# Optimization experiments

Hardware: AMD Instinct MI355X
Metric: run time of the kernel (lower is better)

Reference implementation:

```python
import math
import jax, jax.numpy as jnp
import numpy as np

B, C, T, H, FC, L, K, S, O = 4, 512, 2048, 8, 2048, 6, 3, 256, 1
DK = C // H


def _conv1x1(x, w, b):
    # x: (B,Cin,T), w: (Cout,Cin)
    return jnp.einsum('oc,bct->bot', w, x) + b[None, :, None]


def _conv1d(x, w, b, pad):
    # x: (B,Cin,T), w: (Cout,Cin,K), pad: (left,right)
    y = jax.lax.conv_general_dilated(x, w, (1,), [pad],
                                     dimension_numbers=('NCH', 'OIH', 'NCH'))
    return y + b[None, :, None]


def _layernorm_c(x, g, b, eps=1e-5):
    # LayerNorm over channel dim (module transposes to put channels last)
    m = jnp.mean(x, axis=1, keepdims=True)
    v = jnp.mean((x - m) ** 2, axis=1, keepdims=True)
    return (x - m) * jax.lax.rsqrt(v + eps) * g[None, :, None] + b[None, :, None]


def _attention(x, qw, qb, kw, kb, vw, vb, ow, ob, tri):
    b_, c, t = x.shape
    # reshape(b, H, dk, t).transpose(2,3) -> (B,H,T,dk)
    q = _conv1x1(x, qw, qb).reshape(b_, H, DK, t).transpose(0, 1, 3, 2)
    k = _conv1x1(x, kw, kb).reshape(b_, H, DK, t).transpose(0, 1, 3, 2)
    v = _conv1x1(x, vw, vb).reshape(b_, H, DK, t).transpose(0, 1, 3, 2)
    scores = jnp.einsum('bhtd,bhsd->bhts', q, k) / math.sqrt(DK)
    scores = jnp.where(tri, scores, -1e4)  # causal mask, matches Tensor.where(mask, s, -10000)
    p = jax.nn.softmax(scores, axis=-1)
    o = jnp.einsum('bhts,bhsd->bhtd', p, v)
    o = o.transpose(0, 1, 3, 2).reshape(b_, c, t)
    return _conv1x1(o, ow, ob)


def _ffn(x, x_mask, w1, b1, w2, b2):
    # causal FFN: left pad K-1, activation=None -> relu, p_dropout=0
    y = _conv1d(x * x_mask, w1, b1, (K - 1, 0))
    y = jax.nn.relu(y)
    return _conv1d(y * x_mask, w2, b2, (K - 1, 0)) * x_mask


def _forward(x, norm_f0, x_mask, spk_emb,
             prenet_w, prenet_b, f0pre_w, f0pre_b, cond_w, cond_b, proj_w, proj_b,
             qw, qb, kw, kb, vw, vb, ow, ob,
             ln0_g, ln0_b, ln1_g, ln1_b,
             ffn1_w, ffn1_b, ffn2_w, ffn2_b):
    x = jax.lax.stop_gradient(x)  # torch.detach(x)
    x = x + _conv1x1(spk_emb, cond_w, cond_b)
    x = x + _conv1d(norm_f0, f0pre_w, f0pre_b, (1, 1))
    x = _conv1d(x, prenet_w, prenet_b, (1, 1)) * x_mask
    t = x.shape[2]
    tri = jnp.tril(jnp.ones((t, t), dtype=bool))[None, None]  # subsequent_mask
    x = x * x_mask
    for i in range(L):
        y = _attention(x, qw[i], qb[i], kw[i], kb[i], vw[i], vb[i], ow[i], ob[i], tri)
        x = _layernorm_c(x + y, ln0_g[i], ln0_b[i])
        y = _ffn(x, x_mask, ffn1_w[i], ffn1_b[i], ffn2_w[i], ffn2_b[i])
        x = _layernorm_c(x + y, ln1_g[i], ln1_b[i])
    x = x * x_mask
    return _conv1x1(x, proj_w, proj_b) * x_mask


def setup_inputs() -> dict:
    key = jax.random.key(0)
    ks = iter(jax.random.split(key, 40))
    rn = lambda shape, scale: jax.random.normal(next(ks), shape, jnp.float32) * scale
    inp = {
        'x': rn((B, C, T), 1.0),
        'norm_f0': rn((B, 1, T), 1.0),
        'x_mask': jnp.ones((B, 1, T), jnp.float32),
        'spk_emb': rn((B, S, T), 1.0),
        'prenet_w': rn((C, C, K), (C * K) ** -0.5), 'prenet_b': jnp.zeros((C,), jnp.float32),
        'f0pre_w': rn((C, 1, K), K ** -0.5), 'f0pre_b': jnp.zeros((C,), jnp.float32),
        'cond_w': rn((C, S), S ** -0.5), 'cond_b': jnp.zeros((C,), jnp.float32),
        'proj_w': rn((O, C), C ** -0.5), 'proj_b': jnp.zeros((O,), jnp.float32),
        'qw': rn((L, C, C), C ** -0.5), 'qb': jnp.zeros((L, C), jnp.float32),
        'kw': rn((L, C, C), C ** -0.5), 'kb': jnp.zeros((L, C), jnp.float32),
        'vw': rn((L, C, C), C ** -0.5), 'vb': jnp.zeros((L, C), jnp.float32),
        'ow': rn((L, C, C), C ** -0.5), 'ob': jnp.zeros((L, C), jnp.float32),
        'ln0_g': jnp.ones((L, C), jnp.float32), 'ln0_b': jnp.zeros((L, C), jnp.float32),
        'ln1_g': jnp.ones((L, C), jnp.float32), 'ln1_b': jnp.zeros((L, C), jnp.float32),
        'ffn1_w': rn((L, FC, C, K), (C * K) ** -0.5), 'ffn1_b': jnp.zeros((L, FC), jnp.float32),
        'ffn2_w': rn((L, C, FC, K), (FC * K) ** -0.5), 'ffn2_b': jnp.zeros((L, C), jnp.float32),
    }
    return inp


def reference(x, norm_f0, x_mask, spk_emb,
              prenet_w, prenet_b, f0pre_w, f0pre_b, cond_w, cond_b, proj_w, proj_b,
              qw, qb, kw, kb, vw, vb, ow, ob,
              ln0_g, ln0_b, ln1_g, ln1_b,
              ffn1_w, ffn1_b, ffn2_w, ffn2_b):
    return _forward(x, norm_f0, x_mask, spk_emb,
                    prenet_w, prenet_b, f0pre_w, f0pre_b, cond_w, cond_b, proj_w, proj_b,
                    qw, qb, kw, kb, vw, vb, ow, ob,
                    ln0_g, ln0_b, ln1_g, ln1_b,
                    ffn1_w, ffn1_b, ffn2_w, ffn2_b)
```

## Files before the change

### kernel.cpp

```cpp
#include <hip/hip_runtime.h>
#include <cstdint>
#include <cstddef>

#define T_LEN 2048
#define B_SZ 4
#define C_CH 512
#define H_N 8
#define DK_ 64
#define FC_CH 2048
#define L_N 6
#define KW 3
#define S_CH 256

typedef _Float16 h8 __attribute__((ext_vector_type(8)));
typedef _Float16 h4 __attribute__((ext_vector_type(4)));
typedef float floatx4 __attribute__((ext_vector_type(4)));

__global__ __launch_bounds__(256)
void cast_f16(const float* __restrict__ src, _Float16* __restrict__ dst, int n)
{
    int i = blockIdx.x * 256 + threadIdx.x;
    if (i < n) dst[i] = (_Float16)src[i];
}

__global__ __launch_bounds__(256)
void prepack_k3(const float* __restrict__ src, _Float16* __restrict__ dst, int rk)
{
    const int o = blockIdx.x * 256 + threadIdx.x;
    if (o >= rk) return;
    const size_t row = blockIdx.y;
    const int blk = o / 96, rr = o - blk * 96;
    const int k = rr >> 5, cl = rr & 31;
    dst[row * rk + o] = (_Float16)src[row * rk + (size_t)(blk * 32 + cl) * 3 + k];
}

__global__ __launch_bounds__(256)
void prepack_qkv(const float* __restrict__ qw, const float* __restrict__ kw,
                 const float* __restrict__ vw, const float* __restrict__ qb,
                 const float* __restrict__ kb, const float* __restrict__ vb,
                 _Float16* __restrict__ dst, float* __restrict__ bdst)
{
    int i = blockIdx.x * 256 + threadIdx.x;
    const int total = L_N * 1536 * 512;
    if (i < total) {
        int l = i / (1536 * 512);
        int o = i - l * (1536 * 512);
        int m = o >> 9, c = o & 511;
        const float* s = (m < 512) ? qw : ((m < 1024) ? kw : vw);
        dst[i] = (_Float16)s[((size_t)l * 512 + (m & 511)) * 512 + c];
    }
    if (i < L_N * 1536) {
        int l = i / 1536, m = i - l * 1536;
        const float* s = (m < 512) ? qb : ((m < 1024) ? kb : vb);
        bdst[i] = s[l * 512 + (m & 511)];
    }
}

__global__ __launch_bounds__(256)
void transpose_f0(const float* __restrict__ src, _Float16* __restrict__ dst, int Cd,
                  const float* __restrict__ nf0, const float* __restrict__ f0w,
                  const float* __restrict__ f0b, int do_f0)
{
    __shared__ float tile[32][33];
    const int tl = threadIdx.x & 31;
    const int r  = threadIdx.x >> 5;
    const int t00 = blockIdx.x * 32;
    const int c00 = blockIdx.y * 32;
    const int b   = blockIdx.z;
    const float* s0 = src + (size_t)b * Cd * T_LEN;
#pragma unroll
    for (int rr = 0; rr < 4; ++rr) {
        int cl = r + rr * 8;
        tile[cl][tl] = s0[(size_t)(c00 + cl) * T_LEN + t00 + tl];
    }
    __syncthreads();
    _Float16* d0 = dst + (size_t)b * T_LEN * Cd;
    const int cg = c00 + tl;
#pragma unroll
    for (int rr = 0; rr < 4; ++rr) {
        int tlo = r + rr * 8;
        float v = tile[tl][tlo];
        if (do_f0) {
            int tg = t00 + tlo;
            float a = f0b[cg];
#pragma unroll
            for (int k = 0; k < 3; ++k) {
                int gt = tg + k - 1;
                if (gt >= 0 && gt < T_LEN) a += f0w[cg * 3 + k] * nf0[(size_t)b * T_LEN + gt];
            }
            v += a;
        }
        d0[(size_t)(t00 + tlo) * Cd + cg] = (_Float16)v;
    }
}

template<int KK, int OUTMODE, int MT>
__global__ __launch_bounds__(256)
void conv_gemm_mfma(const _Float16* __restrict__ in, const _Float16* __restrict__ Wpk,
                    const float* __restrict__ bias, const _Float16* __restrict__ res,
                    const float* __restrict__ mask, _Float16* __restrict__ out_v,
                    _Float16* __restrict__ out2,
                    int Cin, int out_stride, int pl, int do_relu,
                    int mask_in, int mask_out)
{
    constexpr int CS   = (KK == 3) ? 32 : 64;
    constexpr int NSEC = (KK == 3) ? 3 : 2;
    constexpr int AST  = NSEC * 32 + 8;
    constexpr int HALO = (KK == 3) ? 2 : 0;
    constexpr int RB   = 128 + 2 * HALO;
    constexpr int BST  = CS + 8;
    constexpr int NAH  = NSEC * MT / 64;
    constexpr int SEGW = NSEC * MT / 8;
    constexpr int IM_N = MT / 32;
    constexpr int NTASK = RB * (CS / 16);
    __shared__ _Float16 sA[2][MT * AST];
    __shared__ _Float16 sB[2][RB * BST];

    const int tid = threadIdx.x;
    const int lane = tid & 63;
    const int wid = tid >> 6;
    const int wm = wid >> 1, wt = wid & 1;
    const int r = lane & 15, q4 = lane >> 4;
    const int t0 = blockIdx.x * 128;
    const int m0 = blockIdx.y * MT;
    const int b  = blockIdx.z;
    const float* mk = mask + (size_t)b * T_LEN;

    floatx4 acc[IM_N][4];
#pragma unroll
    for (int i = 0; i < IM_N; ++i)
#pragma unroll
        for (int j = 0; j < 4; ++j)
#pragma unroll
            for (int c = 0; c < 4; ++c) acc[i][j][c] = 0.f;

    const int arow = tid & (MT - 1);
    const int ah0  = (tid / MT) * SEGW;
    const _Float16* ap = Wpk + (size_t)(m0 + arow) * Cin * KK + ah0;

    int brw[2], bcc[2];
    bool bex[2], bval[2];
    _Float16 bm[2];
    const _Float16* bq[2];
    h8 areg[NAH], breg0[2][2], breg1[2][2];
#pragma unroll
    for (int t2 = 0; t2 < 2; ++t2) {
        const int id = tid + t2 * 256;
        bex[t2] = (id < NTASK);
        int row, c16;
        if (KK == 3) { row = id % RB; c16 = (id / RB) * 16; }
        else         { row = id >> 2; c16 = (id & 3) * 16; }
        const int gt = t0 + row - HALO;
        bval[t2] = bex[t2] && gt >= 0 && gt < T_LEN;
        brw[t2] = row; bcc[t2] = c16;
        bm[t2] = (_Float16)((bval[t2] && mask_in) ? mk[gt] : 1.f);
        bq[t2] = in + (size_t)b * T_LEN * Cin + (size_t)gt * Cin + c16;
#pragma unroll
        for (int hh = 0; hh < 2; ++hh)
#pragma unroll
            for (int j = 0; j < 8; ++j) {
                breg0[t2][hh][j] = (_Float16)0.f;
                breg1[t2][hh][j] = (_Float16)0.f;
            }
    }
    const int nch = Cin / CS;

    auto loadA = [&]() {
        ap += CS * KK;
#pragma unroll
        for (int j = 0; j < NAH; ++j) areg[j] = *reinterpret_cast<const h8*>(ap + j * 8);
    };
    auto loadB = [&](h8 (&br)[2][2]) {
#pragma unroll
        for (int t2 = 0; t2 < 2; ++t2)
            if (bval[t2]) {
                br[t2][0] = *reinterpret_cast<const h8*>(bq[t2]);
                br[t2][1] = *reinterpret_cast<const h8*>(bq[t2] + 8);
                bq[t2] += CS;
            }
    };
    auto stage = [&](int pb, h8 (&br)[2][2]) {
#pragma unroll
        for (int j = 0; j < NAH; ++j)
            *reinterpret_cast<h8*>(&sA[pb][arow * AST + ah0 + j * 8]) = areg[j];
#pragma unroll
        for (int t2 = 0; t2 < 2; ++t2)
            if (bex[t2]) {
                *reinterpret_cast<h8*>(&sB[pb][brw[t2] * BST + bcc[t2]]) = br[t2][0] * bm[t2];
                *reinterpret_cast<h8*>(&sB[pb][brw[t2] * BST + bcc[t2] + 8]) = br[t2][1] * bm[t2];
            }
    };

#pragma unroll
    for (int j = 0; j < NAH; ++j) areg[j] = *reinterpret_cast<const h8*>(ap + j * 8);
#pragma unroll
    for (int t2 = 0; t2 < 2; ++t2)
        if (bval[t2]) {
            breg0[t2][0] = *reinterpret_cast<const h8*>(bq[t2]);
            breg0[t2][1] = *reinterpret_cast<const h8*>(bq[t2] + 8);
            breg1[t2][0] = *reinterpret_cast<const h8*>(bq[t2] + CS);
            breg1[t2][1] = *reinterpret_cast<const h8*>(bq[t2] + CS + 8);
            bq[t2] += 2 * CS;
        }
    stage(0, breg0);
    loadA();
    loadB(breg0);
    __syncthreads();

    auto body = [&](int pb, int cc, h8 (&br)[2][2]) {
        h8 af0[IM_N], bf0[4];
#pragma unroll
        for (int im = 0; im < IM_N; ++im)
            af0[im] = *reinterpret_cast<const h8*>(&sA[pb][(wm * (MT / 2) + im * 16 + r) * AST + q4 * 8]);
        {
            const int rb0 = (KK == 3) ? (wt * 64 + r - pl + HALO) : (wt * 64 + r);
#pragma unroll
            for (int jt = 0; jt < 4; ++jt)
                bf0[jt] = *reinterpret_cast<const h8*>(&sB[pb][(rb0 + jt * 16) * BST + q4 * 8]);
        }
        if (cc + 1 < nch) stage(pb ^ 1, br);
        if (cc + 2 < nch) loadA();
        if (cc + 3 < nch) loadB(br);
#pragma unroll
        for (int im = 0; im < IM_N; ++im)
#pragma unroll
            for (int jt = 0; jt < 4; ++jt)
                acc[im][jt] = __builtin_amdgcn_mfma_f32_16x16x32_f16(af0[im], bf0[jt], acc[im][jt], 0, 0, 0);
#pragma unroll
        for (int sec = 1; sec < NSEC; ++sec) {
            h8 af[IM_N], bf[4];
#pragma unroll
            for (int im = 0; im < IM_N; ++im)
                af[im] = *reinterpret_cast<const h8*>(&sA[pb][(wm * (MT / 2) + im * 16 + r) * AST + sec * 32 + q4 * 8]);
            const int rb0 = (KK == 3) ? (wt * 64 + r + sec - pl + HALO) : (wt * 64 + r);
            const int cb0 = (KK == 3) ? 0 : sec * 32;
#pragma unroll
            for (int jt = 0; jt < 4; ++jt)
                bf[jt] = *reinterpret_cast<const h8*>(&sB[pb][(rb0 + jt * 16) * BST + cb0 + q4 * 8]);
#pragma unroll
            for (int im = 0; im < IM_N; ++im)
#pragma unroll
                for (int jt = 0; jt < 4; ++jt)
                    acc[im][jt] = __builtin_amdgcn_mfma_f32_16x16x32_f16(af[im], bf[jt], acc[im][jt], 0, 0, 0);
        }
        __syncthreads();
    };

    for (int ci = 0; ci < nch; ci += 2) {
        body(0, ci, breg1);
        body(1, ci + 1, breg0);
    }

#pragma unroll
    for (int im = 0; im < IM_N; ++im) {
        const int mb = m0 + wm * (MT / 2) + im * 16 + q4 * 4;
        const float4 bv = *reinterpret_cast<const float4*>(&bias[mb]);
#pragma unroll
        for (int jt = 0; jt < 4; ++jt) {
            const int t = t0 + wt * 64 + jt * 16 + r;
            float vv[4];
            vv[0] = acc[im][jt][0] + bv.x;
            vv[1] = acc[im][jt][1] + bv.y;
            vv[2] = acc[im][jt][2] + bv.z;
            vv[3] = acc[im][jt][3] + bv.w;
            if (do_relu) {
#pragma unroll
                for (int c = 0; c < 4; ++c) vv[c] = fmaxf(vv[c], 0.f);
            }
            if (mask_out) {
                const float mv = mk[t];
#pragma unroll
                for (int c = 0; c < 4; ++c) vv[c] *= mv;
            }
            if (OUTMODE == 1) {
                const size_t ob = ((size_t)b * T_LEN + t) * out_stride + mb;
                if (res) {
                    const h4 rv = *reinterpret_cast<const h4*>(&res[ob]);
#pragma unroll
                    for (int c = 0; c < 4; ++c) vv[c] += (float)rv[c];
                }
                h4 hv;
#pragma unroll
                for (int c = 0; c < 4; ++c) hv[c] = (_Float16)vv[c];
                *reinterpret_cast<h4*>(&out_v[ob]) = hv;
            } else {
                if (m0 < 1024) {
                    const size_t ob = ((size_t)b * T_LEN + t) * 1024 + mb;
                    h4 hv;
#pragma unroll
                    for (int c = 0; c < 4; ++c) hv[c] = (_Float16)vv[c];
                    *reinterpret_cast<h4*>(&out_v[ob]) = hv;
                } else {
#pragma unroll
                    for (int reg = 0; reg < 4; ++reg)
                        out2[((size_t)b * C_CH + (mb - 1024) + reg) * T_LEN + t] = (_Float16)vv[reg];
                }
            }
        }
    }
}

__global__ __launch_bounds__(256)
void flash_attn_mfma(const _Float16* __restrict__ qk, const _Float16* __restrict__ vt,
                     _Float16* __restrict__ o)
{
    __shared__ _Float16 sK[64 * 72];
    __shared__ _Float16 sVt[64 * 72];
    __shared__ _Float16 sP[64 * 72];
    const int tid = threadIdx.x;
    const int lane = tid & 63;
    const int w = tid >> 6;
    const int r = lane & 15, q4 = lane >> 4;
    const int qt0 = (int)(31 - blockIdx.x) * 64;
    const int h = blockIdx.y, b = blockIdx.z;
    const size_t tb = (size_t)b * T_LEN;
    const int hq = h * 64, hk = 512 + h * 64;
    const _Float16* vbase = vt + ((size_t)b * C_CH + h * 64) * T_LEN;

    h8 qf[2];
#pragma unroll
    for (int dc = 0; dc < 2; ++dc) {
        h8 t = *reinterpret_cast<const h8*>(
            &qk[(tb + qt0 + w * 16 + r) * 1024 + hq + dc * 32 + q4 * 8]);
        qf[dc] = t * (_Float16)0.125f;
    }

    floatx4 oacc[4];
    float mrow = -__builtin_inff();
    float lrow = 0.f;
#pragma unroll
    for (int jd = 0; jd < 4; ++jd)
#pragma unroll
        for (int c = 0; c < 4; ++c) oacc[jd][c] = 0.f;

    const int qg = qt0 + w * 16 + r;
    const int nk = (qt0 >> 6) + 1;
    for (int kt = 0; kt < nk; ++kt) {
        const int kt0 = kt * 64;
        __syncthreads();
        {
            int row = tid >> 2, c16 = (tid & 3) * 16;
            const _Float16* src = &qk[(tb + kt0 + row) * 1024 + hk + c16];
            *reinterpret_cast<h8*>(&sK[row * 72 + c16]) = *reinterpret_cast<const h8*>(src);
            *reinterpret_cast<h8*>(&sK[row * 72 + c16 + 8]) = *reinterpret_cast<const h8*>(src + 8);
        }
#pragma unroll
        for (int p = 0; p < 2; ++p) {
            int id = p * 256 + tid;
            int d = id >> 3, s8 = (id & 7) * 8;
            *reinterpret_cast<h8*>(&sVt[d * 72 + s8]) =
                *reinterpret_cast<const h8*>(&vbase[(size_t)d * T_LEN + kt0 + s8]);
        }
        __syncthreads();

        floatx4 sacc[4];
#pragma unroll
        for (int js = 0; js < 4; ++js)
#pragma unroll
            for (int c = 0; c < 4; ++c) sacc[js][c] = 0.f;
#pragma unroll
        for (int dc = 0; dc < 2; ++dc) {
            h8 kf[4];
#pragma unroll
            for (int js = 0; js < 4; ++js)
                kf[js] = *reinterpret_cast<const h8*>(&sK[(js * 16 + r) * 72 + dc * 32 + q4 * 8]);
#pragma unroll
            for (int js = 0; js < 4; ++js)
                sacc[js] = __builtin_amdgcn_mfma_f32_16x16x32_f16(kf[js], qf[dc], sacc[js], 0, 0, 0);
        }
#pragma unroll
        for (int js = 0; js < 4; ++js) {
            const int sb = kt0 + js * 16 + q4 * 4;
#pragma unroll
            for (int reg = 0; reg < 4; ++reg)
                if (sb + reg > qg) sacc[js][reg] = -1e4f;
        }
        float mt;
        {
            float a = fmaxf(fmaxf(sacc[0][0], sacc[0][1]), fmaxf(sacc[0][2], sacc[0][3]));
            float bm = fmaxf(fmaxf(sacc[1][0], sacc[1][1]), fmaxf(sacc[1][2], sacc[1][3]));
            float c = fmaxf(fmaxf(sacc[2][0], sacc[2][1]), fmaxf(sacc[2][2], sacc[2][3]));
            float d = fmaxf(fmaxf(sacc[3][0], sacc[3][1]), fmaxf(sacc[3][2], sacc[3][3]));
            mt = fmaxf(fmaxf(a, bm), fmaxf(c, d));
        }
        mt = fmaxf(mt, __shfl_xor(mt, 16));
        mt = fmaxf(mt, __shfl_xor(mt, 32));
        const float mn = fmaxf(mrow, mt);
        const float alpha = __expf(mrow - mn);
        mrow = mn;
        float rs = 0.f;
#pragma unroll
        for (int js = 0; js < 4; ++js)
#pragma unroll
            for (int reg = 0; reg < 4; ++reg) {
                float p = __expf(sacc[js][reg] - mn);
                sacc[js][reg] = p;
                rs += p;
            }
        rs += __shfl_xor(rs, 16);
        rs += __shfl_xor(rs, 32);
        lrow = lrow * alpha + rs;
        float ao[4];
#pragma unroll
        for (int reg = 0; reg < 4; ++reg) ao[reg] = __shfl(alpha, (q4 << 2) + reg, 16);
#pragma unroll
        for (int jd = 0; jd < 4; ++jd)
#pragma unroll
            for (int reg = 0; reg < 4; ++reg) oacc[jd][reg] *= ao[reg];
#pragma unroll
        for (int js = 0; js < 4; ++js) {
            h4 hv;
#pragma unroll
            for (int reg = 0; reg < 4; ++reg) hv[reg] = (_Float16)sacc[js][reg];
            *reinterpret_cast<h4*>(&sP[(w * 16 + r) * 72 + js * 16 + q4 * 4]) = hv;
        }
#pragma unroll
        for (int sc = 0; sc < 2; ++sc) {
            h8 pf = *reinterpret_cast<const h8*>(&sP[(w * 16 + r) * 72 + sc * 32 + q4 * 8]);
            h8 vf[4];
#pragma unroll
            for (int jd = 0; jd < 4; ++jd)
                vf[jd] = *reinterpret_cast<const h8*>(&sVt[(jd * 16 + r) * 72 + sc * 32 + q4 * 8]);
#pragma unroll
            for (int jd = 0; jd < 4; ++jd)
                oacc[jd] = __builtin_amdgcn_mfma_f32_16x16x32_f16(pf, vf[jd], oacc[jd], 0, 0, 0);
        }
    }
    const float linv = 1.f / lrow;
    float li[4];
#pragma unroll
    for (int reg = 0; reg < 4; ++reg) li[reg] = __shfl(linv, (q4 << 2) + reg, 16);
#pragma unroll
    for (int reg = 0; reg < 4; ++reg) {
        const size_t rowb = (tb + qt0 + w * 16 + (q4 << 2) + reg) * 512 + h * 64 + r;
#pragma unroll
        for (int jd = 0; jd < 4; ++jd)
            o[rowb + jd * 16] = (_Float16)(oacc[jd][reg] * li[reg]);
    }
}

__global__ __launch_bounds__(256)
void ln_kernel(const _Float16* __restrict__ x, const _Float16* __restrict__ y,
               const float* __restrict__ g, const float* __restrict__ be,
               _Float16* __restrict__ outx)
{
    const int w = threadIdx.x >> 6, lane = threadIdx.x & 63;
    const int t = blockIdx.x * 4 + w, b = blockIdx.y;
    const size_t base = ((size_t)b * T_LEN + t) * C_CH + lane * 8;
    h8 xv = *reinterpret_cast<const h8*>(&x[base]);
    h8 yv = *reinterpret_cast<const h8*>(&y[base]);
    float v[8];
#pragma unroll
    for (int i = 0; i < 8; ++i) v[i] = (float)xv[i] + (float)yv[i];
    float s = 0.f, s2 = 0.f;
#pragma unroll
    for (int i = 0; i < 8; ++i) { s += v[i]; s2 += v[i] * v[i]; }
#pragma unroll
    for (int off = 1; off < 64; off <<= 1) {
        s  += __shfl_xor(s, off);
        s2 += __shfl_xor(s2, off);
    }
    const float mean = s * (1.f / C_CH);
    const float var  = s2 * (1.f / C_CH) - mean * mean;
    const float rstd = rsqrtf(var + 1e-5f);
    float4 g0 = *reinterpret_cast<const float4*>(&g[lane * 8]);
    float4 g1 = *reinterpret_cast<const float4*>(&g[lane * 8 + 4]);
    float4 b0 = *reinterpret_cast<const float4*>(&be[lane * 8]);
    float4 b1 = *reinterpret_cast<const float4*>(&be[lane * 8 + 4]);
    const float gg[8] = {g0.x, g0.y, g0.z, g0.w, g1.x, g1.y, g1.z, g1.w};
    const float bb[8] = {b0.x, b0.y, b0.z, b0.w, b1.x, b1.y, b1.z, b1.w};
    h8 ov;
#pragma unroll
    for (int i = 0; i < 8; ++i)
        ov[i] = (_Float16)((v[i] - mean) * rstd * gg[i] + bb[i]);
    *reinterpret_cast<h8*>(&outx[base]) = ov;
}

__global__ __launch_bounds__(256)
void proj_kernel(const _Float16* __restrict__ x, const float* __restrict__ pw,
                 const float* __restrict__ pb, const float* __restrict__ mask,
                 float* __restrict__ out)
{
    const int w = threadIdx.x >> 6, lane = threadIdx.x & 63;
    const int t = blockIdx.x * 4 + w, b = blockIdx.y;
    const size_t base = ((size_t)b * T_LEN + t) * C_CH + lane * 8;
    h8 xv = *reinterpret_cast<const h8*>(&x[base]);
    float4 p0 = *reinterpret_cast<const float4*>(&pw[lane * 8]);
    float4 p1 = *reinterpret_cast<const float4*>(&pw[lane * 8 + 4]);
    const float pp[8] = {p0.x, p0.y, p0.z, p0.w, p1.x, p1.y, p1.z, p1.w};
    float s = 0.f;
#pragma unroll
    for (int i = 0; i < 8; ++i) s += (float)xv[i] * pp[i];
#pragma unroll
    for (int off = 1; off < 64; off <<= 1) s += __shfl_xor(s, off);
    if (lane == 0) {
        const float mv = mask[(size_t)b * T_LEN + t];
        out[(size_t)b * T_LEN + t] = (s * mv + pb[0]) * mv;
    }
}

extern "C" void kernel_launch(void* const* d_in, const int* in_sizes, int n_in,
                              void* d_out, int out_size, void* d_ws, size_t ws_size,
                              hipStream_t stream)
{
    const float* x    = (const float*)d_in[0];
    const float* nf0  = (const float*)d_in[1];
    const float* xm   = (const float*)d_in[2];
    const float* spk  = (const float*)d_in[3];
    const float* prw  = (const float*)d_in[4];
    const float* prb  = (const float*)d_in[5];
    const float* f0w  = (const float*)d_in[6];
    const float* f0b  = (const float*)d_in[7];
    const float* cw   = (const float*)d_in[8];
    const float* cb   = (const float*)d_in[9];
    const float* pjw  = (const float*)d_in[10];
    const float* pjb  = (const float*)d_in[11];
    const float* qw   = (const float*)d_in[12];
    const float* qb   = (const float*)d_in[13];
    const float* kw   = (const float*)d_in[14];
    const float* kb   = (const float*)d_in[15];
    const float* vw   = (const float*)d_in[16];
    const float* vb   = (const float*)d_in[17];
    const float* ow   = (const float*)d_in[18];
    const float* ob   = (const float*)d_in[19];
    const float* ln0g = (const float*)d_in[20];
    const float* ln0b = (const float*)d_in[21];
    const float* ln1g = (const float*)d_in[22];
    const float* ln1b = (const float*)d_in[23];
    const float* f1w  = (const float*)d_in[24];
    const float* f1b  = (const float*)d_in[25];
    const float* f2w  = (const float*)d_in[26];
    const float* f2b  = (const float*)d_in[27];
    float* out = (float*)d_out;

    const size_t NCT = (size_t)B_SZ * C_CH * T_LEN;
    char* wp = (char*)d_ws;
    _Float16* xbuf = (_Float16*)wp; wp += NCT * 2;
    _Float16* t0h  = (_Float16*)wp; wp += NCT * 2;
    _Float16* qk   = (_Float16*)wp; wp += NCT * 4;
    _Float16* vt   = (_Float16*)wp; wp += NCT * 2;
    _Float16* obf  = (_Float16*)wp; wp += NCT * 2;
    _Float16* h1   = (_Float16*)wp; wp += NCT * 8;
    _Float16* xT   = h1;
    _Float16* spkT = obf;
    _Float16* Wqkv = (_Float16*)wp; wp += (size_t)L_N * 1536 * 512 * 2;
    _Float16* Wo   = (_Float16*)wp; wp += (size_t)L_N * 512 * 512 * 2;
    _Float16* Wcnd = (_Float16*)wp; wp += (size_t)512 * 256 * 2;
    _Float16* Wpre = (_Float16*)wp; wp += (size_t)512 * 512 * 3 * 2;
    _Float16* Wf1  = (_Float16*)wp; wp += (size_t)L_N * 2048 * 512 * 3 * 2;
    _Float16* Wf2  = (_Float16*)wp; wp += (size_t)L_N * 512 * 2048 * 3 * 2;
    float*    Bqkv = (float*)wp;    wp += (size_t)L_N * 1536 * 4;

    dim3 blk(256);
    dim3 gC64(16, 8, B_SZ);
    dim3 gQKV(16, 24, B_SZ);
    dim3 gF(16, 32, B_SZ);
    dim3 gAT(32, H_N, B_SZ);
    dim3 gLN(T_LEN / 4, B_SZ);

    {
        int n;
        n = C_CH * S_CH;       cast_f16<<<(n + 255) / 256, blk, 0, stream>>>(cw, Wcnd, n);
        n = L_N * C_CH * C_CH; cast_f16<<<(n + 255) / 256, blk, 0, stream>>>(ow, Wo, n);
        prepack_k3<<<dim3(6, C_CH), blk, 0, stream>>>(prw, Wpre, C_CH * 3);
        prepack_k3<<<dim3(6, L_N * FC_CH), blk, 0, stream>>>(f1w, Wf1, C_CH * 3);
        prepack_k3<<<dim3(24, L_N * C_CH), blk, 0, stream>>>(f2w, Wf2, FC_CH * 3);
        n = L_N * 1536 * 512;  prepack_qkv<<<(n + 255) / 256, blk, 0, stream>>>(qw, kw, vw, qb, kb, vb, Wqkv, Bqkv);
    }

    transpose_f0<<<dim3(64, 16, B_SZ), blk, 0, stream>>>(x, xT, C_CH, nf0, f0w, f0b, 1);
    transpose_f0<<<dim3(64, 8, B_SZ), blk, 0, stream>>>(spk, spkT, S_CH, nullptr, nullptr, nullptr, 0);
    conv_gemm_mfma<1, 1, 64><<<gC64, blk, 0, stream>>>(spkT, Wcnd, cb, xT, xm, t0h, nullptr, S_CH, C_CH, 0, 0, 0, 0);
    conv_gemm_mfma<3, 1, 64><<<gC64, blk, 0, stream>>>(t0h, Wpre, prb, nullptr, xm, xbuf, nullptr, C_CH, C_CH, 1, 0, 0, 1);

    for (int l = 0; l < L_N; ++l) {
        const size_t bo = (size_t)l * C_CH;
        conv_gemm_mfma<1, 3, 64><<<gQKV, blk, 0, stream>>>(xbuf, Wqkv + (size_t)l * 1536 * 512, Bqkv + l * 1536,
                                                           nullptr, xm, qk, vt, C_CH, 1024, 0, 0, 0, 0);
        flash_attn_mfma<<<gAT, blk, 0, stream>>>(qk, vt, obf);
        conv_gemm_mfma<1, 1, 64><<<gC64, blk, 0, stream>>>(obf, Wo + (size_t)l * 512 * 512, ob + bo,
                                                           nullptr, xm, t0h, nullptr, C_CH, C_CH, 0, 0, 0, 0);
        ln_kernel<<<gLN, blk, 0, stream>>>(xbuf, t0h, ln0g + bo, ln0b + bo, xbuf);
        conv_gemm_mfma<3, 1, 64><<<gF, blk, 0, stream>>>(xbuf, Wf1 + (size_t)l * FC_CH * C_CH * 3, f1b + (size_t)l * FC_CH,
                                                         nullptr, xm, h1, nullptr, C_CH, FC_CH, 2, 1, 1, 0);
        conv_gemm_mfma<3, 1, 64><<<gC64, blk, 0, stream>>>(h1, Wf2 + (size_t)l * C_CH * FC_CH * 3, f2b + bo,
                                                           nullptr, xm, t0h, nullptr, FC_CH, C_CH, 2, 0, 1, 1);
        ln_kernel<<<gLN, blk, 0, stream>>>(xbuf, t0h, ln1g + bo, ln1b + bo, xbuf);
    }
    proj_kernel<<<gLN, blk, 0, stream>>>(xbuf, pjw, pjb, xm, out);
}
```

Before: 2.223 ms.

## Add single-buffered MT=128 GEMM variant for QKV and FFN1 convolutions

Adds a DBUF template parameter to the conv GEMM. With DBUF=0 it uses one shared-memory buffer, with a sync-stage-sync pattern per chunk and register prefetch of the next chunk. The QKV and FFN1 launches switch to a 128-row M tile with half the grid in y, so each block reuses the B tile over twice as many output channels. The single LDS buffer keeps shared memory within limits at the larger tile, but it gives up the LDS double buffering, adds an extra barrier per chunk, and doubles the accumulator registers.

Result: faster. 2.167 ms (-2.5%).

```diff
diff --git a/kernel.cpp b/kernel.cpp
--- a/kernel.cpp
+++ b/kernel.cpp
@@ -94,7 +94,7 @@
     }
 }
 
-template<int KK, int OUTMODE, int MT>
+template<int KK, int OUTMODE, int MT, int DBUF>
 __global__ __launch_bounds__(256)
 void conv_gemm_mfma(const _Float16* __restrict__ in, const _Float16* __restrict__ Wpk,
                     const float* __restrict__ bias, const _Float16* __restrict__ res,
@@ -113,8 +113,9 @@
     constexpr int SEGW = NSEC * MT / 8;
     constexpr int IM_N = MT / 32;
     constexpr int NTASK = RB * (CS / 16);
-    __shared__ _Float16 sA[2][MT * AST];
-    __shared__ _Float16 sB[2][RB * BST];
+    constexpr int NBUF = DBUF + 1;
+    __shared__ _Float16 sA[NBUF][MT * AST];
+    __shared__ _Float16 sB[NBUF][RB * BST];
 
     const int tid = threadIdx.x;
     const int lane = tid & 63;
@@ -202,53 +203,86 @@
             breg1[t2][1] = *reinterpret_cast<const h8*>(bq[t2] + CS + 8);
             bq[t2] += 2 * CS;
         }
-    stage(0, breg0);
-    loadA();
-    loadB(breg0);
-    __syncthreads();
-
-    auto body = [&](int pb, int cc, h8 (&br)[2][2]) {
-        h8 af0[IM_N], bf0[4];
-#pragma unroll
-        for (int im = 0; im < IM_N; ++im)
-            af0[im] = *reinterpret_cast<const h8*>(&sA[pb][(wm * (MT / 2) + im * 16 + r) * AST + q4 * 8]);
-        {
-            const int rb0 = (KK == 3) ? (wt * 64 + r - pl + HALO) : (wt * 64 + r);
-#pragma unroll
-            for (int jt = 0; jt < 4; ++jt)
-                bf0[jt] = *reinterpret_cast<const h8*>(&sB[pb][(rb0 + jt * 16) * BST + q4 * 8]);
-        }
-        if (cc + 1 < nch) stage(pb ^ 1, br);
-        if (cc + 2 < nch) loadA();
-        if (cc + 3 < nch) loadB(br);
-#pragma unroll
-        for (int im = 0; im < IM_N; ++im)
-#pragma unroll
-            for (int jt = 0; jt < 4; ++jt)
-                acc[im][jt] = __builtin_amdgcn_mfma_f32_16x16x32_f16(af0[im], bf0[jt], acc[im][jt], 0, 0, 0);
-#pragma unroll
-        for (int sec = 1; sec < NSEC; ++sec) {
-            h8 af[IM_N], bf[4];
+
+    if constexpr (DBUF == 1) {
+        stage(0, breg0);
+        loadA();
+        loadB(breg0);
+        __syncthreads();
+
+        auto body = [&](int pb, int cc, h8 (&br)[2][2]) {
+            h8 af0[IM_N], bf0[4];
 #pragma unroll
             for (int im = 0; im < IM_N; ++im)
-                af[im] = *reinterpret_cast<const h8*>(&sA[pb][(wm * (MT / 2) + im * 16 + r) * AST + sec * 32 + q4 * 8]);
-            const int rb0 = (KK == 3) ? (wt * 64 + r + sec - pl + HALO) : (wt * 64 + r);
-            const int cb0 = (KK == 3) ? 0 : sec * 32;
-#pragma unroll
-            for (int jt = 0; jt < 4; ++jt)
-                bf[jt] = *reinterpret_cast<const h8*>(&sB[pb][(rb0 + jt * 16) * BST + cb0 + q4 * 8]);
+                af0[im] = *reinterpret_cast<const h8*>(&sA[pb][(wm * (MT / 2) + im * 16 + r) * AST + q4 * 8]);
+            {
+                const int rb0 = (KK == 3) ? (wt * 64 + r - pl + HALO) : (wt * 64 + r);
+#pragma unroll
+                for (int jt = 0; jt < 4; ++jt)
+                    bf0[jt] = *reinterpret_cast<const h8*>(&sB[pb][(rb0 + jt * 16) * BST + q4 * 8]);
+            }
+            if (cc + 1 < nch) stage(pb ^ 1, br);
+            if (cc + 2 < nch) loadA();
+            if (cc + 3 < nch) loadB(br);
 #pragma unroll
             for (int im = 0; im < IM_N; ++im)
 #pragma unroll
                 for (int jt = 0; jt < 4; ++jt)
-                    acc[im][jt] = __builtin_amdgcn_mfma_f32_16x16x32_f16(af[im], bf[jt], acc[im][jt], 0, 0, 0);
-        }
-        __syncthreads();
-    };
-
-    for (int ci = 0; ci < nch; ci += 2) {
-        body(0, ci, breg1);
-        body(1, ci + 1, breg0);
+                    acc[im][jt] = __builtin_amdgcn_mfma_f32_16x16x32_f16(af0[im], bf0[jt], acc[im][jt], 0, 0, 0);
+#pragma unroll
+            for (int sec = 1; sec < NSEC; ++sec) {
+                h8 af[IM_N], bf[4];
+#pragma unroll
+                for (int im = 0; im < IM_N; ++im)
+                    af[im] = *reinterpret_cast<const h8*>(&sA[pb][(wm * (MT / 2) + im * 16 + r) * AST + sec * 32 + q4 * 8]);
+                const int rb0 = (KK == 3) ? (wt * 64 + r + sec - pl + HALO) : (wt * 64 + r);
+                const int cb0 = (KK == 3) ? 0 : sec * 32;
+#pragma unroll
+                for (int jt = 0; jt < 4; ++jt)
+                    bf[jt] = *reinterpret_cast<const h8*>(&sB[pb][(rb0 + jt * 16) * BST + cb0 + q4 * 8]);
+#pragma unroll
+                for (int im = 0; im < IM_N; ++im)
+#pragma unroll
+                    for (int jt = 0; jt < 4; ++jt)
+                        acc[im][jt] = __builtin_amdgcn_mfma_f32_16x16x32_f16(af[im], bf[jt], acc[im][jt], 0, 0, 0);
+            }
+            __syncthreads();
+        };
+
+        for (int ci = 0; ci < nch; ci += 2) {
+            body(0, ci, breg1);
+            body(1, ci + 1, breg0);
+        }
+    } else {
+        auto run_chunk = [&](h8 (&br)[2][2], int ci) {
+            __syncthreads();
+            stage(0, br);
+            __syncthreads();
+            if (ci + 1 < nch) loadA();
+            if (ci + 2 < nch) loadB(br);
+#pragma unroll
+            for (int sec = 0; sec < NSEC; ++sec) {
+                h8 af[IM_N], bf[4];
+#pragma unroll
+                for (int im = 0; im < IM_N; ++im)
+                    af[im] = *reinterpret_cast<const h8*>(&sA[0][(wm * (MT / 2) + im * 16 + r) * AST + sec * 32 + q4 * 8]);
+                const int rb0 = (KK == 3) ? (wt * 64 + r + sec - pl + HALO) : (wt * 64 + r);
+                const int cb0 = (KK == 3) ? 0 : sec * 32;
+#pragma unroll
+                for (int jt = 0; jt < 4; ++jt)
+                    bf[jt] = *reinterpret_cast<const h8*>(&sB[0][(rb0 + jt * 16) * BST + cb0 + q4 * 8]);
+#pragma unroll
+                for (int im = 0; im < IM_N; ++im)
+#pragma unroll
+                    for (int jt = 0; jt < 4; ++jt)
+                        acc[im][jt] = __builtin_amdgcn_mfma_f32_16x16x32_f16(af[im], bf[jt], acc[im][jt], 0, 0, 0);
+            }
+        };
+
+        for (int ci = 0; ci < nch; ci += 2) {
+            run_chunk(breg0, ci);
+            run_chunk(breg1, ci + 1);
+        }
     }
 
 #pragma unroll
@@ -553,8 +587,8 @@
 
     dim3 blk(256);
     dim3 gC64(16, 8, B_SZ);
-    dim3 gQKV(16, 24, B_SZ);
-    dim3 gF(16, 32, B_SZ);
+    dim3 gQKV(16, 12, B_SZ);
+    dim3 gF(16, 16, B_SZ);
     dim3 gAT(32, H_N, B_SZ);
     dim3 gLN(T_LEN / 4, B_SZ);
 
@@ -570,21 +604,21 @@
 
     transpose_f0<<<dim3(64, 16, B_SZ), blk, 0, stream>>>(x, xT, C_CH, nf0, f0w, f0b, 1);
     transpose_f0<<<dim3(64, 8, B_SZ), blk, 0, stream>>>(spk, spkT, S_CH, nullptr, nullptr, nullptr, 0);
-    conv_gemm_mfma<1, 1, 64><<<gC64, blk, 0, stream>>>(spkT, Wcnd, cb, xT, xm, t0h, nullptr, S_CH, C_CH, 0, 0, 0, 0);
-    conv_gemm_mfma<3, 1, 64><<<gC64, blk, 0, stream>>>(t0h, Wpre, prb, nullptr, xm, xbuf, nullptr, C_CH, C_CH, 1, 0, 0, 1);
+    conv_gemm_mfma<1, 1, 64, 1><<<gC64, blk, 0, stream>>>(spkT, Wcnd, cb, xT, xm, t0h, nullptr, S_CH, C_CH, 0, 0, 0, 0);
+    conv_gemm_mfma<3, 1, 64, 1><<<gC64, blk, 0, stream>>>(t0h, Wpre, prb, nullptr, xm, xbuf, nullptr, C_CH, C_CH, 1, 0, 0, 1);
 
     for (int l = 0; l < L_N; ++l) {
         const size_t bo = (size_t)l * C_CH;
-        conv_gemm_mfma<1, 3, 64><<<gQKV, blk, 0, stream>>>(xbuf, Wqkv + (size_t)l * 1536 * 512, Bqkv + l * 1536,
-                                                           nullptr, xm, qk, vt, C_CH, 1024, 0, 0, 0, 0);
+        conv_gemm_mfma<1, 3, 128, 0><<<gQKV, blk, 0, stream>>>(xbuf, Wqkv + (size_t)l * 1536 * 512, Bqkv + l * 1536,
+                                                               nullptr, xm, qk, vt, C_CH, 1024, 0, 0, 0, 0);
         flash_attn_mfma<<<gAT, blk, 0, stream>>>(qk, vt, obf);
-        conv_gemm_mfma<1, 1, 64><<<gC64, blk, 0, stream>>>(obf, Wo + (size_t)l * 512 * 512, ob + bo,
-                                                           nullptr, xm, t0h, nullptr, C_CH, C_CH, 0, 0, 0, 0);
+        conv_gemm_mfma<1, 1, 64, 1><<<gC64, blk, 0, stream>>>(obf, Wo + (size_t)l * 512 * 512, ob + bo,
+                                                              nullptr, xm, t0h, nullptr, C_CH, C_CH, 0, 0, 0, 0);
         ln_kernel<<<gLN, blk, 0, stream>>>(xbuf, t0h, ln0g + bo, ln0b + bo, xbuf);
-        conv_gemm_mfma<3, 1, 64><<<gF, blk, 0, stream>>>(xbuf, Wf1 + (size_t)l * FC_CH * C_CH * 3, f1b + (size_t)l * FC_CH,
-                                                         nullptr, xm, h1, nullptr, C_CH, FC_CH, 2, 1, 1, 0);
-        conv_gemm_mfma<3, 1, 64><<<gC64, blk, 0, stream>>>(h1, Wf2 + (size_t)l * C_CH * FC_CH * 3, f2b + bo,
-                                                           nullptr, xm, t0h, nullptr, FC_CH, C_CH, 2, 0, 1, 1);
+        conv_gemm_mfma<3, 1, 128, 0><<<gF, blk, 0, stream>>>(xbuf, Wf1 + (size_t)l * FC_CH * C_CH * 3, f1b + (size_t)l * FC_CH,
+                                                             nullptr, xm, h1, nullptr, C_CH, FC_CH, 2, 1, 1, 0);
+        conv_gemm_mfma<3, 1, 64, 1><<<gC64, blk, 0, stream>>>(h1, Wf2 + (size_t)l * C_CH * FC_CH * 3, f2b + bo,
+                                                              nullptr, xm, t0h, nullptr, FC_CH, C_CH, 2, 0, 1, 1);
         ln_kernel<<<gLN, blk, 0, stream>>>(xbuf, t0h, ln1g + bo, ln1b + bo, xbuf);
     }
     proj_kernel<<<gLN, blk, 0, stream>>>(xbuf, pjw, pjb, xm, out);
```

## Load weight fragments directly to registers, bypass LDS; use 128-row tiles

Applied to the files above, without the earlier changes.

The conv GEMM kernel no longer stages the weight (A) tile through shared memory. Each lane now loads its MFMA A fragments straight from global memory into double-buffered registers, prefetched two chunks ahead. This removes LDS stores, LDS reads and part of the shared-memory footprint. The QKV, FFN1 and FFN2 GEMMs switch to MT=128 tiles with halved grid sizes, which raises reuse of the input tile but increases register pressure (up to 2×12 h8 fragments for KK=3) and cuts the block count, notably for FFN2 (256 blocks).

Result: slower. 2.735 ms (+23.1%).

```diff
diff --git a/kernel.cpp b/kernel.cpp
--- a/kernel.cpp
+++ b/kernel.cpp
@@ -105,15 +105,12 @@
 {
     constexpr int CS   = (KK == 3) ? 32 : 64;
     constexpr int NSEC = (KK == 3) ? 3 : 2;
-    constexpr int AST  = NSEC * 32 + 8;
     constexpr int HALO = (KK == 3) ? 2 : 0;
     constexpr int RB   = 128 + 2 * HALO;
     constexpr int BST  = CS + 8;
-    constexpr int NAH  = NSEC * MT / 64;
-    constexpr int SEGW = NSEC * MT / 8;
     constexpr int IM_N = MT / 32;
+    constexpr int NFR  = IM_N * NSEC;
     constexpr int NTASK = RB * (CS / 16);
-    __shared__ _Float16 sA[2][MT * AST];
     __shared__ _Float16 sB[2][RB * BST];
 
     const int tid = threadIdx.x;
@@ -134,15 +131,23 @@
 #pragma unroll
             for (int c = 0; c < 4; ++c) acc[i][j][c] = 0.f;
 
-    const int arow = tid & (MT - 1);
-    const int ah0  = (tid / MT) * SEGW;
-    const _Float16* ap = Wpk + (size_t)(m0 + arow) * Cin * KK + ah0;
+    const _Float16* afp = Wpk + (size_t)(m0 + wm * (MT / 2) + r) * (Cin * KK) + q4 * 8;
+    h8 afA[NFR], afB[NFR];
+    auto loadAF = [&](h8 (&af)[NFR]) {
+#pragma unroll
+        for (int im = 0; im < IM_N; ++im)
+#pragma unroll
+            for (int sec = 0; sec < NSEC; ++sec)
+                af[im * NSEC + sec] =
+                    *reinterpret_cast<const h8*>(afp + (size_t)im * 16 * Cin * KK + sec * 32);
+        afp += CS * KK;
+    };
 
     int brw[2], bcc[2];
     bool bex[2], bval[2];
     _Float16 bm[2];
     const _Float16* bq[2];
-    h8 areg[NAH], breg0[2][2], breg1[2][2];
+    h8 breg0[2][2], breg1[2][2];
 #pragma unroll
     for (int t2 = 0; t2 < 2; ++t2) {
         const int id = tid + t2 * 256;
@@ -165,11 +170,6 @@
     }
     const int nch = Cin / CS;
 
-    auto loadA = [&]() {
-        ap += CS * KK;
-#pragma unroll
-        for (int j = 0; j < NAH; ++j) areg[j] = *reinterpret_cast<const h8*>(ap + j * 8);
-    };
     auto loadB = [&](h8 (&br)[2][2]) {
 #pragma unroll
         for (int t2 = 0; t2 < 2; ++t2)
@@ -179,10 +179,7 @@
                 bq[t2] += CS;
             }
     };
-    auto stage = [&](int pb, h8 (&br)[2][2]) {
-#pragma unroll
-        for (int j = 0; j < NAH; ++j)
-            *reinterpret_cast<h8*>(&sA[pb][arow * AST + ah0 + j * 8]) = areg[j];
+    auto stageB = [&](int pb, h8 (&br)[2][2]) {
 #pragma unroll
         for (int t2 = 0; t2 < 2; ++t2)
             if (bex[t2]) {
@@ -191,8 +188,8 @@
             }
     };
 
-#pragma unroll
-    for (int j = 0; j < NAH; ++j) areg[j] = *reinterpret_cast<const h8*>(ap + j * 8);
+    loadAF(afA);
+    loadAF(afB);
 #pragma unroll
     for (int t2 = 0; t2 < 2; ++t2)
         if (bval[t2]) {
@@ -202,36 +199,28 @@
             breg1[t2][1] = *reinterpret_cast<const h8*>(bq[t2] + CS + 8);
             bq[t2] += 2 * CS;
         }
-    stage(0, breg0);
-    loadA();
+    stageB(0, breg0);
     loadB(breg0);
     __syncthreads();
 
-    auto body = [&](int pb, int cc, h8 (&br)[2][2]) {
-        h8 af0[IM_N], bf0[4];
-#pragma unroll
-        for (int im = 0; im < IM_N; ++im)
-            af0[im] = *reinterpret_cast<const h8*>(&sA[pb][(wm * (MT / 2) + im * 16 + r) * AST + q4 * 8]);
+    auto body = [&](int pb, int cc, h8 (&br)[2][2], h8 (&af)[NFR]) {
+        h8 bf0[4];
         {
             const int rb0 = (KK == 3) ? (wt * 64 + r - pl + HALO) : (wt * 64 + r);
 #pragma unroll
             for (int jt = 0; jt < 4; ++jt)
                 bf0[jt] = *reinterpret_cast<const h8*>(&sB[pb][(rb0 + jt * 16) * BST + q4 * 8]);
         }
-        if (cc + 1 < nch) stage(pb ^ 1, br);
-        if (cc + 2 < nch) loadA();
+        if (cc + 1 < nch) stageB(pb ^ 1, br);
         if (cc + 3 < nch) loadB(br);
 #pragma unroll
         for (int im = 0; im < IM_N; ++im)
 #pragma unroll
             for (int jt = 0; jt < 4; ++jt)
-                acc[im][jt] = __builtin_amdgcn_mfma_f32_16x16x32_f16(af0[im], bf0[jt], acc[im][jt], 0, 0, 0);
+                acc[im][jt] = __builtin_amdgcn_mfma_f32_16x16x32_f16(af[im * NSEC], bf0[jt], acc[im][jt], 0, 0, 0);
 #pragma unroll
         for (int sec = 1; sec < NSEC; ++sec) {
-            h8 af[IM_N], bf[4];
-#pragma unroll
-            for (int im = 0; im < IM_N; ++im)
-                af[im] = *reinterpret_cast<const h8*>(&sA[pb][(wm * (MT / 2) + im * 16 + r) * AST + sec * 32 + q4 * 8]);
+            h8 bf[4];
             const int rb0 = (KK == 3) ? (wt * 64 + r + sec - pl + HALO) : (wt * 64 + r);
             const int cb0 = (KK == 3) ? 0 : sec * 32;
 #pragma unroll
@@ -241,14 +230,15 @@
             for (int im = 0; im < IM_N; ++im)
 #pragma unroll
                 for (int jt = 0; jt < 4; ++jt)
-                    acc[im][jt] = __builtin_amdgcn_mfma_f32_16x16x32_f16(af[im], bf[jt], acc[im][jt], 0, 0, 0);
-        }
+                    acc[im][jt] = __builtin_amdgcn_mfma_f32_16x16x32_f16(af[im * NSEC + sec], bf[jt], acc[im][jt], 0, 0, 0);
+        }
+        if (cc + 2 < nch) loadAF(af);
         __syncthreads();
     };
 
     for (int ci = 0; ci < nch; ci += 2) {
-        body(0, ci, breg1);
-        body(1, ci + 1, breg0);
+        body(0, ci, breg1, afA);
+        body(1, ci + 1, breg0, afB);
     }
 
 #pragma unroll
@@ -553,8 +543,9 @@
 
     dim3 blk(256);
     dim3 gC64(16, 8, B_SZ);
-    dim3 gQKV(16, 24, B_SZ);
-    dim3 gF(16, 32, B_SZ);
+    dim3 gF2(16, 4, B_SZ);
+    dim3 gQKV(16, 12, B_SZ);
+    dim3 gF(16, 16, B_SZ);
     dim3 gAT(32, H_N, B_SZ);
     dim3 gLN(T_LEN / 4, B_SZ);
 
@@ -575,15 +566,15 @@
 
     for (int l = 0; l < L_N; ++l) {
         const size_t bo = (size_t)l * C_CH;
-        conv_gemm_mfma<1, 3, 64><<<gQKV, blk, 0, stream>>>(xbuf, Wqkv + (size_t)l * 1536 * 512, Bqkv + l * 1536,
-                                                           nullptr, xm, qk, vt, C_CH, 1024, 0, 0, 0, 0);
+        conv_gemm_mfma<1, 3, 128><<<gQKV, blk, 0, stream>>>(xbuf, Wqkv + (size_t)l * 1536 * 512, Bqkv + l * 1536,
+                                                            nullptr, xm, qk, vt, C_CH, 1024, 0, 0, 0, 0);
         flash_attn_mfma<<<gAT, blk, 0, stream>>>(qk, vt, obf);
         conv_gemm_mfma<1, 1, 64><<<gC64, blk, 0, stream>>>(obf, Wo + (size_t)l * 512 * 512, ob + bo,
                                                            nullptr, xm, t0h, nullptr, C_CH, C_CH, 0, 0, 0, 0);
         ln_kernel<<<gLN, blk, 0, stream>>>(xbuf, t0h, ln0g + bo, ln0b + bo, xbuf);
-        conv_gemm_mfma<3, 1, 64><<<gF, blk, 0, stream>>>(xbuf, Wf1 + (size_t)l * FC_CH * C_CH * 3, f1b + (size_t)l * FC_CH,
-                                                         nullptr, xm, h1, nullptr, C_CH, FC_CH, 2, 1, 1, 0);
-        conv_gemm_mfma<3, 1, 64><<<gC64, blk, 0, stream>>>(h1, Wf2 + (size_t)l * C_CH * FC_CH * 3, f2b + bo,
+        conv_gemm_mfma<3, 1, 128><<<gF, blk, 0, stream>>>(xbuf, Wf1 + (size_t)l * FC_CH * C_CH * 3, f1b + (size_t)l * FC_CH,
+                                                          nullptr, xm, h1, nullptr, C_CH, FC_CH, 2, 1, 1, 0);
+        conv_gemm_mfma<3, 1, 128><<<gF2, blk, 0, stream>>>(h1, Wf2 + (size_t)l * C_CH * FC_CH * 3, f2b + bo,
                                                            nullptr, xm, t0h, nullptr, FC_CH, C_CH, 2, 0, 1, 1);
         ln_kernel<<<gLN, blk, 0, stream>>>(xbuf, t0h, ln1g + bo, ln1b + bo, xbuf);
     }
```
